# Optimization experiments

Measured on AMD Instinct MI355X. Metric: run time of the kernel, lower is better.

Reference implementation:

```python
import jax, jax.numpy as jnp
import numpy as np

WS = 32          # window_size
STRIDE = 16
OUTPUT = 224
GRADE_N = 6

def _dct_mat(size):
    i = np.arange(size)[:, None]
    j = np.arange(size)[None, :]
    scale = np.where(i == 0, np.sqrt(1.0 / size), np.sqrt(2.0 / size))
    return (scale * np.cos((j + 0.5) * np.pi * i / size)).astype(np.float32)

def _gen_filter(start, end, size):
    i = np.arange(size)[:, None]
    j = np.arange(size)[None, :]
    s = i + j
    return np.where((s > end) | (s < start), 0.0, 1.0).astype(np.float32)

# constant (non-learnable) buffers, derived from init hyperparams
_D = jnp.asarray(_dct_mat(WS))                       # [32,32]
_LEVEL_FILT = jnp.asarray(_gen_filter(0, WS * 2, WS))  # level_fliter=[0] -> band (0, 64)
_grade_filts = np.stack([_gen_filter(WS * 2.0 / GRADE_N * i, WS * 2.0 / GRADE_N * (i + 1), WS)
                         for i in range(GRADE_N)])    # [G,32,32]
_ft_num = _grade_filts.sum(axis=(1, 2))               # per-filter normalizer
_weights = (2.0 ** np.arange(GRADE_N)).astype(np.float32)  # w=1, *=2 each pass
_GRADE_FILT_SCALED = jnp.asarray(_grade_filts * (_weights / _ft_num)[:, None, None])  # [G,32,32]

def _unfold(x):
    # x: [B,C,H,W] -> patches [B,L,C,ws,ws], L row-major over (oh, ow), matching torch Unfold
    B, C, H, W = x.shape
    nH = (H - WS) // STRIDE + 1
    nW = (W - WS) // STRIDE + 1
    r = jnp.arange(nH) * STRIDE
    c = jnp.arange(nW) * STRIDE
    rows = r[:, None, None, None] + jnp.arange(WS)[None, None, :, None]  # [nH,1,ws,1]
    cols = c[None, :, None, None] + jnp.arange(WS)[None, None, None, :]  # [1,nW,1,ws]
    p = x[:, :, rows, cols]                       # [B,C,nH,nW,ws,ws]
    p = jnp.transpose(p, (0, 2, 3, 1, 4, 5))      # [B,nH,nW,C,ws,ws]
    return p.reshape(B, nH * nW, C, WS, WS)

def setup_inputs() -> dict:
    key = jax.random.key(0)
    x = jax.random.normal(key, (16, 3, 512, 512), dtype=jnp.float32)
    return {"x": x}

def reference(x):
    B, C, H, W = x.shape
    patches = _unfold(x)                          # [B,L,C,32,32]
    x_dct = _D @ patches @ _D.T                   # batched 32x32 DCT

    # level branch (level_N=1): filter is all-pass band (0,64) but applied faithfully
    level_y = _D.T @ (x_dct * _LEVEL_FILT) @ _D   # [B,L,C,32,32]

    # grading: sum_g w_g/ft_g * sum_{c,i,j} filt_g * log(|dct|+1)
    lx = jnp.log(jnp.abs(x_dct) + 1.0)
    grade = jnp.einsum('blcij,gij->bl', lx, _GRADE_FILT_SCALED)  # [B,L]

    idx = jnp.argsort(grade, axis=-1)             # ascending
    b = jnp.arange(B)
    minmin_i  = idx[:, 0]
    minmin_i1 = idx[:, 1]    # B > 1 branch
    maxmax_i  = idx[:, -1]
    maxmax_i1 = idx[:, -2]   # B > 1 branch

    # gather single patch per image; fold0 with one block == reshape to [B,C,32,32]
    x_minmin  = level_y[b, minmin_i]
    x_maxmax  = level_y[b, maxmax_i]
    x_minmin1 = level_y[b, minmin_i1]
    x_maxmax1 = level_y[b, maxmax_i1]
    return (x_minmin, x_maxmax, x_minmin1, x_maxmax1)
```

## Files before the change

kernel.cpp:

```cpp
#include <hip/hip_runtime.h>
#include <cstdint>

constexpr double kPI  = 3.14159265358979323846264338327950288;
constexpr double kLN2 = 0.69314718055994530941723212145818;
constexpr double cos_poly(double x) {
    double x2 = x * x, term = 1.0, sum = 1.0;
    for (int n = 1; n <= 13; ++n) { term *= -x2 / double((2 * n - 1) * (2 * n)); sum += term; }
    return sum;
}
constexpr double cos_idx(int a) {
    a &= 127;
    if (a <= 32)  return  cos_poly(a * kPI / 64.0);
    if (a <= 64)  return -cos_poly((64 - a) * kPI / 64.0);
    if (a <= 96)  return -cos_poly((a - 64) * kPI / 64.0);
    return cos_poly((128 - a) * kPI / 64.0);
}
constexpr double csqrt(double v) {
    double x = 1.0;
    for (int i = 0; i < 60; ++i) x = 0.5 * (x + v / x);
    return x;
}
constexpr float Dij(int i, int j) {
    double sc = (i == 0) ? csqrt(1.0 / 32.0) : 0.25;
    int a = ((2 * j + 1) * i) & 127;
    return (float)(sc * cos_idx(a));
}
struct OddT { float d[256]; };
constexpr OddT make_odd() { OddT t{}; for (int m = 0; m < 16; ++m) for (int k = 0; k < 16; ++k) t.d[m*16+k] = Dij(2*m+1, k); return t; }
struct E8T { float d[64]; };
constexpr E8T make_e2() { E8T t{}; for (int m = 0; m < 8; ++m) for (int k = 0; k < 8; ++k) t.d[m*8+k] = Dij(4*m+2, k); return t; }
struct E4T { float d[16]; };
constexpr E4T make_ee() { E4T t{}; for (int m = 0; m < 4; ++m) for (int k = 0; k < 4; ++k) t.d[m*4+k] = Dij(8*m,   k); return t; }
constexpr E4T make_eo() { E4T t{}; for (int m = 0; m < 4; ++m) for (int k = 0; k < 4; ++k) t.d[m*4+k] = Dij(8*m+4, k); return t; }
struct FTab { float f[64]; };
constexpr FTab make_F() {
    FTab t{};
    const int lo[6] = {0, 11, 22, 32, 43, 54};
    const int hi[6] = {10, 21, 32, 42, 53, 62};
    const int n [6] = {66, 187, 306, 286, 165, 45};
    for (int s = 0; s < 64; ++s) {
        double acc = 0.0, w = 1.0;
        for (int g = 0; g < 6; ++g) { if (s >= lo[g] && s <= hi[g]) acc += w / double(n[g]); w *= 2.0; }
        t.f[s] = (float)(acc * kLN2);
    }
    return t;
}
__device__ constexpr OddT cOdd = make_odd();
__device__ constexpr E8T  cE2  = make_e2();
__device__ constexpr E4T  cEE  = make_ee();
__device__ constexpr E4T  cEO  = make_eo();
__device__ constexpr FTab cF   = make_F();

#define NP  15376
#define LPB 961
#define SST 36

template <typename EMIT>
__device__ __forceinline__ void dct32(const float* __restrict__ v, EMIT&& emit) {
    float e[16], o[16];
    #pragma unroll
    for (int k = 0; k < 16; ++k) { e[k] = v[k] + v[31-k]; o[k] = v[k] - v[31-k]; }
    float ee[8], eo[8];
    #pragma unroll
    for (int k = 0; k < 8; ++k)  { ee[k] = e[k] + e[15-k]; eo[k] = e[k] - e[15-k]; }
    float eee[4], eeo[4];
    #pragma unroll
    for (int k = 0; k < 4; ++k)  { eee[k] = ee[k] + ee[7-k]; eeo[k] = ee[k] - ee[7-k]; }
    #pragma unroll
    for (int m = 0; m < 16; m += 2) {
        float a = 0.f, b = 0.f;
        #pragma unroll
        for (int k = 0; k < 16; ++k) {
            a = fmaf(cOdd.d[m*16+k],     o[k], a);
            b = fmaf(cOdd.d[(m+1)*16+k], o[k], b);
        }
        emit(2*m+1, a); emit(2*m+3, b);
    }
    #pragma unroll
    for (int m = 0; m < 8; m += 2) {
        float a = 0.f, b = 0.f;
        #pragma unroll
        for (int k = 0; k < 8; ++k) {
            a = fmaf(cE2.d[m*8+k],     eo[k], a);
            b = fmaf(cE2.d[(m+1)*8+k], eo[k], b);
        }
        emit(4*m+2, a); emit(4*m+6, b);
    }
    {
        float a0=0.f,a1=0.f,a2=0.f,a3=0.f,b0=0.f,b1=0.f,b2=0.f,b3=0.f;
        #pragma unroll
        for (int k = 0; k < 4; ++k) {
            a0 = fmaf(cEE.d[0*4+k], eee[k], a0);
            a1 = fmaf(cEE.d[1*4+k], eee[k], a1);
            a2 = fmaf(cEE.d[2*4+k], eee[k], a2);
            a3 = fmaf(cEE.d[3*4+k], eee[k], a3);
            b0 = fmaf(cEO.d[0*4+k], eeo[k], b0);
            b1 = fmaf(cEO.d[1*4+k], eeo[k], b1);
            b2 = fmaf(cEO.d[2*4+k], eeo[k], b2);
            b3 = fmaf(cEO.d[3*4+k], eeo[k], b3);
        }
        emit(0, a0); emit(8, a1); emit(16, a2); emit(24, a3);
        emit(4, b0); emit(12, b1); emit(20, b2); emit(28, b3);
    }
}

__global__ __launch_bounds__(128) void k_grade(const float* __restrict__ x,
                                               float* __restrict__ partial) {
    __shared__ __align__(16) float sS[4][32 * SST];
    __shared__ float sF[64];
    const int tid = threadIdx.x, g = tid >> 5, lane = tid & 31;
    if (tid < 64) sF[tid] = cF.f[tid];

    const int task = blockIdx.x * 4 + g;
    const int b  = task / LPB;
    const int l  = task - b * LPB;
    const int ph = l / 31, pw = l - ph * 31;
    const float* cb = x + (size_t)(b * 3) * 262144 + (ph * 16) * 512 + pw * 16 + lane * 512;
    float* S = sS[g];
    __syncthreads();

    float w[32];
    #pragma unroll
    for (int i = 0; i < 32; ++i) w[i] = sF[lane + i];

    float4 cur[8];
    #pragma unroll
    for (int q = 0; q < 8; ++q) cur[q] = ((const float4*)cb)[q];

    float gsum = 0.0f;
    #pragma unroll 1
    for (int c = 0; c < 3; ++c) {
        float p[32];
        #pragma unroll
        for (int q = 0; q < 8; ++q) {
            float4 f = cur[q];
            p[4*q] = f.x; p[4*q+1] = f.y; p[4*q+2] = f.z; p[4*q+3] = f.w;
        }
        if (c < 2) {
            cb += 262144;
            #pragma unroll
            for (int q = 0; q < 8; ++q) cur[q] = ((const float4*)cb)[q];
        }
        dct32(p, [&](int j, float acc) { S[j * SST + lane] = acc; });
        __syncthreads();

        float u[32];
        #pragma unroll
        for (int q = 0; q < 8; ++q) {
            float4 uu = *(const float4*)&S[lane * SST + 4 * q];
            u[4*q] = uu.x; u[4*q+1] = uu.y; u[4*q+2] = uu.z; u[4*q+3] = uu.w;
        }
        __syncthreads();
        dct32(u, [&](int i, float z) {
            gsum = fmaf(__log2f(fabsf(z) + 1.0f), w[i], gsum);
        });
    }
    #pragma unroll
    for (int off = 16; off > 0; off >>= 1) gsum += __shfl_down(gsum, off, 32);
    if (lane == 0) partial[task] = gsum;
}

__global__ __launch_bounds__(256) void k_selgather(const float* __restrict__ partial,
                                                   const float* __restrict__ x,
                                                   float* __restrict__ out) {
    __shared__ unsigned long long smx1[256], smx2[256], smn1[256], smn2[256];
    __shared__ int ssel[4];
    const int b = blockIdx.x, tid = threadIdx.x;
    unsigned long long mx1 = 0, mx2 = 0, mn1 = ~0ULL, mn2 = ~0ULL;
    for (int l = tid; l < LPB; l += 256) {
        unsigned int bits = __float_as_uint(partial[b * LPB + l]);
        unsigned long long k = ((unsigned long long)bits << 32) | (unsigned int)l;
        if (k > mx1) { mx2 = mx1; mx1 = k; } else if (k > mx2) { mx2 = k; }
        if (k < mn1) { mn2 = mn1; mn1 = k; } else if (k < mn2) { mn2 = k; }
    }
    smx1[tid] = mx1; smx2[tid] = mx2; smn1[tid] = mn1; smn2[tid] = mn2;
    for (int off = 128; off > 0; off >>= 1) {
        __syncthreads();
        if (tid < off) {
            unsigned long long a1 = smx1[tid], a2 = smx2[tid], b1 = smx1[tid + off], b2 = smx2[tid + off];
            unsigned long long lo = a1 < b1 ? a1 : b1, hi = a1 < b1 ? b1 : a1;
            unsigned long long c2 = a2 > b2 ? a2 : b2;
            smx1[tid] = hi; smx2[tid] = lo > c2 ? lo : c2;
            a1 = smn1[tid]; a2 = smn2[tid]; b1 = smn1[tid + off]; b2 = smn2[tid + off];
            lo = a1 < b1 ? a1 : b1; hi = a1 < b1 ? b1 : a1;
            c2 = a2 < b2 ? a2 : b2;
            smn1[tid] = lo; smn2[tid] = hi < c2 ? hi : c2;
        }
    }
    __syncthreads();
    if (tid == 0) {
        ssel[0] = (int)(smn1[0] & 0xffffffffu);
        ssel[1] = (int)(smx1[0] & 0xffffffffu);
        ssel[2] = (int)(smn2[0] & 0xffffffffu);
        ssel[3] = (int)(smx2[0] & 0xffffffffu);
    }
    __syncthreads();

    #pragma unroll
    for (int it = 0; it < 12; ++it) {
        const int q  = it * 256 + tid;
        const int o  = q / 768;
        const int r2 = q - o * 768;
        const int c  = r2 >> 8;
        const int p  = r2 & 255;
        const int i  = p >> 3, j4 = p & 7;
        const int l  = ssel[o];
        const int r0 = (l / 31) * 16, c0 = (l - (l / 31) * 31) * 16;
        const float4 v = *(const float4*)(x + ((size_t)(b * 3 + c) * 512 + r0 + i) * 512 + c0 + 4 * j4);
        *(float4*)(out + (size_t)o * 49152 + b * 3072 + c * 1024 + i * 32 + 4 * j4) = v;
    }
}

extern "C" void kernel_launch(void* const* d_in, const int* in_sizes, int n_in,
                              void* d_out, int out_size, void* d_ws, size_t ws_size,
                              hipStream_t stream) {
    const float* x = (const float*)d_in[0];
    float* out     = (float*)d_out;
    float* partial = (float*)d_ws;
    k_grade    <<<NP / 4, 128, 0, stream>>>(x, partial);
    k_selgather<<<16,     256, 0, stream>>>(partial, x, out);
}
```

Before: 112.0 us.

## Split grading work per channel across warps and sum channels in selection

Each 32-lane group now handles one (patch, channel) pair instead of looping over all three channels, so the launch covers three times as many tasks. Blocks shrink to 64 threads. The per-channel partial sums are written separately and added in the selection kernel. This raises parallelism and removes the serial channel loop and its double-buffered prefetch, but it drops cross-channel load overlap, adds global partial traffic, and changes the shared-memory padding to 34, which forces float2 instead of float4 reads.

```diff
diff --git a/kernel.cpp b/kernel.cpp
--- a/kernel.cpp
+++ b/kernel.cpp
@@ -52,8 +52,9 @@
 __device__ constexpr FTab cF   = make_F();
 
 #define NP  15376
+#define NPC 46128
 #define LPB 961
-#define SST 36
+#define SST 34
 
 template <typename EMIT>
 __device__ __forceinline__ void dct32(const float* __restrict__ v, EMIT&& emit) {
@@ -104,60 +105,44 @@
     }
 }
 
-__global__ __launch_bounds__(128) void k_grade(const float* __restrict__ x,
-                                               float* __restrict__ partial) {
-    __shared__ __align__(16) float sS[4][32 * SST];
+__global__ __launch_bounds__(64) void k_grade(const float* __restrict__ x,
+                                              float* __restrict__ partial) {
+    __shared__ __align__(16) float sS[2][32 * SST];
     __shared__ float sF[64];
     const int tid = threadIdx.x, g = tid >> 5, lane = tid & 31;
-    if (tid < 64) sF[tid] = cF.f[tid];
-
-    const int task = blockIdx.x * 4 + g;
+    sF[tid] = cF.f[tid];
+
+    const int tc   = blockIdx.x * 2 + g;
+    const int task = tc / 3, c = tc - task * 3;
     const int b  = task / LPB;
     const int l  = task - b * LPB;
     const int ph = l / 31, pw = l - ph * 31;
-    const float* cb = x + (size_t)(b * 3) * 262144 + (ph * 16) * 512 + pw * 16 + lane * 512;
+    const float4* row = (const float4*)(x + (size_t)(b * 3 + c) * 262144
+                                          + (ph * 16 + lane) * 512 + pw * 16);
     float* S = sS[g];
+
+    float p[32];
+    #pragma unroll
+    for (int q = 0; q < 8; ++q) {
+        float4 f = row[q];
+        p[4*q] = f.x; p[4*q+1] = f.y; p[4*q+2] = f.z; p[4*q+3] = f.w;
+    }
+    dct32(p, [&](int j, float acc) { S[j * SST + lane] = acc; });
     __syncthreads();
 
-    float w[32];
-    #pragma unroll
-    for (int i = 0; i < 32; ++i) w[i] = sF[lane + i];
-
-    float4 cur[8];
-    #pragma unroll
-    for (int q = 0; q < 8; ++q) cur[q] = ((const float4*)cb)[q];
-
+    float u[32];
+    #pragma unroll
+    for (int h = 0; h < 16; ++h) {
+        float2 uu = *(const float2*)&S[lane * SST + 2 * h];
+        u[2*h] = uu.x; u[2*h+1] = uu.y;
+    }
     float gsum = 0.0f;
-    #pragma unroll 1
-    for (int c = 0; c < 3; ++c) {
-        float p[32];
-        #pragma unroll
-        for (int q = 0; q < 8; ++q) {
-            float4 f = cur[q];
-            p[4*q] = f.x; p[4*q+1] = f.y; p[4*q+2] = f.z; p[4*q+3] = f.w;
-        }
-        if (c < 2) {
-            cb += 262144;
-            #pragma unroll
-            for (int q = 0; q < 8; ++q) cur[q] = ((const float4*)cb)[q];
-        }
-        dct32(p, [&](int j, float acc) { S[j * SST + lane] = acc; });
-        __syncthreads();
-
-        float u[32];
-        #pragma unroll
-        for (int q = 0; q < 8; ++q) {
-            float4 uu = *(const float4*)&S[lane * SST + 4 * q];
-            u[4*q] = uu.x; u[4*q+1] = uu.y; u[4*q+2] = uu.z; u[4*q+3] = uu.w;
-        }
-        __syncthreads();
-        dct32(u, [&](int i, float z) {
-            gsum = fmaf(__log2f(fabsf(z) + 1.0f), w[i], gsum);
-        });
-    }
+    dct32(u, [&](int i, float z) {
+        gsum = fmaf(__log2f(fabsf(z) + 1.0f), sF[i + lane], gsum);
+    });
     #pragma unroll
     for (int off = 16; off > 0; off >>= 1) gsum += __shfl_down(gsum, off, 32);
-    if (lane == 0) partial[task] = gsum;
+    if (lane == 0) partial[tc] = gsum;
 }
 
 __global__ __launch_bounds__(256) void k_selgather(const float* __restrict__ partial,
@@ -168,7 +153,9 @@
     const int b = blockIdx.x, tid = threadIdx.x;
     unsigned long long mx1 = 0, mx2 = 0, mn1 = ~0ULL, mn2 = ~0ULL;
     for (int l = tid; l < LPB; l += 256) {
-        unsigned int bits = __float_as_uint(partial[b * LPB + l]);
+        const float* pp = partial + (size_t)(b * LPB + l) * 3;
+        float gr = pp[0] + pp[1] + pp[2];
+        unsigned int bits = __float_as_uint(gr);
         unsigned long long k = ((unsigned long long)bits << 32) | (unsigned int)l;
         if (k > mx1) { mx2 = mx1; mx1 = k; } else if (k > mx2) { mx2 = k; }
         if (k < mn1) { mn2 = mn1; mn1 = k; } else if (k < mn2) { mn2 = k; }
@@ -217,6 +204,6 @@
     const float* x = (const float*)d_in[0];
     float* out     = (float*)d_out;
     float* partial = (float*)d_ws;
-    k_grade    <<<NP / 4, 128, 0, stream>>>(x, partial);
+    k_grade    <<<NPC / 2, 64, 0, stream>>>(x, partial);
     k_selgather<<<16,     256, 0, stream>>>(partial, x, out);
 }
```

Measured after the change: 111.3 us. No clear change (-0.6%).
